# Kernel optimization log

Hardware: AMD Instinct MI355X
Metric: run time of the kernel (lower is better)

## Reference

```python
import jax, jax.numpy as jnp
import numpy as np
import math

EMBED_DIM = 1024
N_HEADS = 16
HEAD_DIM = EMBED_DIM // N_HEADS
B, N = 2, 2048


def setup_inputs() -> dict:
    key = jax.random.key(0)
    k1, k2, k3 = jax.random.split(key, 3)
    x = jax.random.normal(k1, (B, N, EMBED_DIM), dtype=jnp.float32)
    # Per-head Linear(D, 3*head_dim), stacked over heads. PyTorch Linear init scale ~1/sqrt(fan_in).
    bound = 1.0 / math.sqrt(EMBED_DIM)
    Wkqv = jax.random.uniform(k2, (N_HEADS, EMBED_DIM, 3 * HEAD_DIM), dtype=jnp.float32, minval=-bound, maxval=bound)
    bkqv = jax.random.uniform(k3, (N_HEADS, 3 * HEAD_DIM), dtype=jnp.float32, minval=-bound, maxval=bound)
    return {"x": x, "Wkqv": Wkqv, "bkqv": bkqv}


def reference(x, Wkqv, bkqv):
    Bx, Nx, D = x.shape
    hd = Wkqv.shape[-1] // 3
    # all heads at once: [B, H, N, 3*hd]
    proj = jnp.einsum('bnd,hdf->bhnf', x, Wkqv) + bkqv[None, :, None, :]
    # torch.split order in the original is (k, q, v)
    k, q, v = jnp.split(proj, 3, axis=-1)
    # scores = q @ k^T / sqrt(head_dim)   [B, H, N, N]
    scores = jnp.einsum('bhqd,bhkd->bhqk', q, k) / math.sqrt(hd)
    causal = jnp.tril(jnp.ones((Nx, Nx), dtype=bool))
    scores = jnp.where(causal[None, None, :, :], scores, -jnp.inf)
    attn = jax.nn.softmax(scores, axis=-1)
    out = jnp.einsum('bhqk,bhkd->bhqd', attn, v)  # [B, H, N, hd]
    # concat heads -> [B, N, D]  (forward() passes no out_matrix, so no output projection)
    return out.transpose(0, 2, 1, 3).reshape(Bx, Nx, D)
```

## Files before the change

kernel.cpp:

```cpp
#include <hip/hip_runtime.h>
#include <math.h>

typedef float f32x4 __attribute__((ext_vector_type(4)));
typedef __bf16 bf16x8 __attribute__((ext_vector_type(8)));

#define MFMA16(a, b, c) __builtin_amdgcn_mfma_f32_16x16x32_bf16((a), (b), (c), 0, 0, 0)

constexpr int Bsz = 2, Nseq = 2048, Dm = 1024, Hh = 16, HDim = 64, F3 = 192;
constexpr int Mrows = Bsz * Nseq;
constexpr int NC = Hh * F3;
constexpr float QSCALE = 0.125f * 1.4426950408889634f;

__device__ inline void load_lds16(const void* g, void* l) {
    __builtin_amdgcn_global_load_lds((const __attribute__((address_space(1))) void*)g,
                                     (__attribute__((address_space(3))) void*)l, 16, 0, 0);
}

#define FENCE asm volatile("" ::: "memory")
#define BARRIER do { FENCE; __builtin_amdgcn_s_barrier(); FENCE; } while (0)
#define WAIT6 asm volatile("s_waitcnt vmcnt(6)" ::: "memory")

__global__ __launch_bounds__(256) void conv_x_kernel(const float* __restrict__ x,
                                                     __bf16* __restrict__ xb) {
    int i = blockIdx.x * 256 + threadIdx.x;
    const float4* xv = reinterpret_cast<const float4*>(x);
    float4 a = xv[2 * i];
    float4 b = xv[2 * i + 1];
    bf16x8 o = {(__bf16)a.x, (__bf16)a.y, (__bf16)a.z, (__bf16)a.w,
                (__bf16)b.x, (__bf16)b.y, (__bf16)b.z, (__bf16)b.w};
    *reinterpret_cast<bf16x8*>(xb + 8 * i) = o;
}

__global__ __launch_bounds__(256) void conv_w_kernel(const float* __restrict__ w,
                                                     __bf16* __restrict__ wt) {
    __shared__ __bf16 tile[32][66];
    int h = blockIdx.z, d0 = blockIdx.x * 32, c0 = blockIdx.y * 64;
    for (int i = threadIdx.x; i < 32 * 64; i += 256) {
        int di = i >> 6, cj = i & 63;
        tile[di][cj] = (__bf16)w[(size_t)(h * Dm + d0 + di) * F3 + c0 + cj];
    }
    __syncthreads();
    for (int i = threadIdx.x; i < 32 * 64; i += 256) {
        int ci = i >> 5, dj = i & 31;
        wt[(size_t)(h * F3 + c0 + ci) * Dm + d0 + dj] = tile[dj][ci];
    }
}

__global__ __launch_bounds__(512, 2) void gemm_proj(const __bf16* __restrict__ xb,
                                                    const __bf16* __restrict__ wt,
                                                    const float* __restrict__ bias,
                                                    __bf16* __restrict__ kbuf,
                                                    __bf16* __restrict__ qbuf,
                                                    __bf16* __restrict__ vt) {
    __shared__ __align__(16) __bf16 Ab[2][256 * 64];
    __shared__ __align__(16) __bf16 Bb[2][256 * 64];

    int flat = blockIdx.x;
    int swz = (flat & 7) * 24 + (flat >> 3);
    int bm = swz / 12, bn = swz % 12;
    int r0 = bm * 256, n0 = bn * 256;

    int w = threadIdx.x >> 6, lane = threadIdx.x & 63;
    int col = lane & 15, quad = lane >> 4;
    int wm = w >> 2, wn = w & 3;

    f32x4 acc[8][4] = {};
    bf16x8 af[2][4];
    bf16x8 bfr[2][2];

    auto stageA = [&](int t, int s, int h) {
        int rl = lane >> 3;
        int cg = (lane & 7) ^ rl;
#pragma unroll
        for (int r = 0; r < 2; r++) {
            int rowb = r * 128 + h * 64 + w * 8;
            load_lds16(xb + (size_t)(r0 + rowb + rl) * Dm + t * 64 + cg * 8,
                       &Ab[s][rowb * 64]);
        }
    };
    auto stageB = [&](int t, int s, int h) {
        int rl = lane >> 3;
        int cg = (lane & 7) ^ rl;
#pragma unroll
        for (int r = 0; r < 2; r++) {
            int rowb = ((w >> 2) + r * 2) * 64 + h * 32 + (w & 3) * 8;
            load_lds16(wt + (size_t)(n0 + rowb + rl) * Dm + t * 64 + cg * 8,
                       &Bb[s][rowb * 64]);
        }
    };

    auto readA = [&](int s, int mh) {
#pragma unroll
        for (int ks = 0; ks < 2; ks++)
#pragma unroll
            for (int mt = 0; mt < 4; mt++) {
                int row = wm * 128 + mh * 64 + mt * 16 + col;
                af[ks][mt] = *reinterpret_cast<const bf16x8*>(
                    &Ab[s][row * 64 + (((ks * 4 + quad) ^ (row & 7)) * 8)]);
            }
    };
    auto readB = [&](int s, int nh) {
#pragma unroll
        for (int ks = 0; ks < 2; ks++)
#pragma unroll
            for (int nt = 0; nt < 2; nt++) {
                int row = wn * 64 + nh * 32 + nt * 16 + col;
                bfr[ks][nt] = *reinterpret_cast<const bf16x8*>(
                    &Bb[s][row * 64 + (((ks * 4 + quad) ^ (row & 7)) * 8)]);
            }
    };
    auto mfmaQ = [&](int mh, int nh) {
        __builtin_amdgcn_s_setprio(1);
#pragma unroll
        for (int ks = 0; ks < 2; ks++)
#pragma unroll
            for (int mt = 0; mt < 4; mt++)
#pragma unroll
                for (int nt = 0; nt < 2; nt++)
                    acc[mh * 4 + mt][nh * 2 + nt] =
                        MFMA16(af[ks][mt], bfr[ks][nt], acc[mh * 4 + mt][nh * 2 + nt]);
        __builtin_amdgcn_s_setprio(0);
    };

    stageA(0, 0, 0); stageB(0, 0, 0); stageA(0, 0, 1); stageB(0, 0, 1);
    stageA(1, 1, 0);
    stageB(1, 1, 0); stageA(1, 1, 1);
    WAIT6;
    BARRIER;

    for (int i = 0; i < 8; i++) {
        int t0 = 2 * i;
        int t2 = t0 + 2; if (t2 > 15) t2 = 15;
        int t3 = t0 + 3; if (t3 > 15) t3 = 15;

        readA(0, 0); readB(0, 0);
        stageB(t0 + 1, 1, 1);
        BARRIER; mfmaQ(0, 0); BARRIER;

        readB(0, 1);
        stageA(t2, 0, 0);
        BARRIER; mfmaQ(0, 1); BARRIER;

        readA(0, 1); readB(0, 0);
        BARRIER; mfmaQ(1, 0); BARRIER;

        readB(0, 1);
        stageB(t2, 0, 0); stageA(t2, 0, 1);
        WAIT6;
        BARRIER; mfmaQ(1, 1); BARRIER;

        readA(1, 0); readB(1, 0);
        stageB(t2, 0, 1);
        BARRIER; mfmaQ(0, 0); BARRIER;

        readB(1, 1);
        stageA(t3, 1, 0);
        BARRIER; mfmaQ(0, 1); BARRIER;

        readA(1, 1); readB(1, 0);
        BARRIER; mfmaQ(1, 0); BARRIER;

        readB(1, 1);
        stageB(t3, 1, 0); stageA(t3, 1, 1);
        WAIT6;
        BARRIER; mfmaQ(1, 1); BARRIER;
    }

#pragma unroll
    for (int nt = 0; nt < 4; nt++) {
        int g = n0 + wn * 64 + nt * 16 + col;
        int h = g / F3, c = g - h * F3;
        float bv = bias[g];
        bool isq = (c >= 64 && c < 128), isv = (c >= 128);
        int cd = c & 63;
#pragma unroll
        for (int mt = 0; mt < 8; mt++) {
#pragma unroll
            for (int rg = 0; rg < 4; rg++) {
                int r = r0 + wm * 128 + mt * 16 + quad * 4 + rg;
                int b = r >> 11, n = r & (Nseq - 1);
                float v = acc[mt][nt][rg] + bv;
                if (isq) v *= QSCALE;
                size_t bh = (size_t)(b * Hh + h);
                if (isv) vt[(bh * HDim + cd) * Nseq + n] = (__bf16)v;
                else ((isq) ? qbuf : kbuf)[(bh * Nseq + n) * HDim + cd] = (__bf16)v;
            }
        }
    }
}

__global__ __launch_bounds__(256) void proj_small(const float* __restrict__ x,
                                                  const __bf16* __restrict__ wt,
                                                  const float* __restrict__ bias,
                                                  __bf16* __restrict__ kbuf,
                                                  __bf16* __restrict__ qbuf,
                                                  __bf16* __restrict__ vt) {
    int h = blockIdx.y;
    int wave = threadIdx.x >> 6, lane = threadIdx.x & 63;
    int col = lane & 15, quad = lane >> 4;
    int r0 = blockIdx.x * 128 + wave * 32;

    f32x4 acc[12][2] = {};
    const float* xr0 = x + (size_t)(r0 + col) * Dm + quad * 8;
    const float* xr1 = xr0 + 16 * Dm;
    const __bf16* wbase = wt + (size_t)(h * F3 + col) * Dm + quad * 8;

    for (int k0 = 0; k0 < Dm; k0 += 32) {
        float4 a0lo = *reinterpret_cast<const float4*>(xr0 + k0);
        float4 a0hi = *reinterpret_cast<const float4*>(xr0 + k0 + 4);
        float4 a1lo = *reinterpret_cast<const float4*>(xr1 + k0);
        float4 a1hi = *reinterpret_cast<const float4*>(xr1 + k0 + 4);
        bf16x8 a0 = {(__bf16)a0lo.x, (__bf16)a0lo.y, (__bf16)a0lo.z, (__bf16)a0lo.w,
                     (__bf16)a0hi.x, (__bf16)a0hi.y, (__bf16)a0hi.z, (__bf16)a0hi.w};
        bf16x8 a1 = {(__bf16)a1lo.x, (__bf16)a1lo.y, (__bf16)a1lo.z, (__bf16)a1lo.w,
                     (__bf16)a1hi.x, (__bf16)a1hi.y, (__bf16)a1hi.z, (__bf16)a1hi.w};
#pragma unroll
        for (int ct = 0; ct < 12; ct++) {
            bf16x8 bf = *reinterpret_cast<const bf16x8*>(wbase + ct * 16 * Dm + k0);
            acc[ct][0] = MFMA16(a0, bf, acc[ct][0]);
            acc[ct][1] = MFMA16(a1, bf, acc[ct][1]);
        }
    }
#pragma unroll
    for (int ct = 0; ct < 12; ct++) {
        int c = ct * 16 + col;
        float bv = bias[h * F3 + c];
        int cd = c & 63;
        bool isq = (c >= 64 && c < 128), isv = (c >= 128);
#pragma unroll
        for (int rt = 0; rt < 2; rt++) {
#pragma unroll
            for (int rg = 0; rg < 4; rg++) {
                int r = r0 + rt * 16 + quad * 4 + rg;
                int b = r >> 11, n = r & (Nseq - 1);
                float v = acc[ct][rt][rg] + bv;
                if (isq) v *= QSCALE;
                size_t bh = (size_t)(b * Hh + h);
                if (isv) vt[(bh * HDim + cd) * Nseq + n] = (__bf16)v;
                else ((isq) ? qbuf : kbuf)[(bh * Nseq + n) * HDim + cd] = (__bf16)v;
            }
        }
    }
}

__global__ __launch_bounds__(512) void attn_kernel(const __bf16* __restrict__ qbuf,
                                                   const __bf16* __restrict__ kbuf,
                                                   const __bf16* __restrict__ vt,
                                                   float* __restrict__ out) {
    __shared__ __align__(16) __bf16 Kb[64 * 64];
    __shared__ __align__(16) __bf16 Vb[64 * 64];
    __shared__ __align__(16) __bf16 plds[8][16][72];
    int bh = blockIdx.x;
    int b = bh >> 4, h = bh & 15;
    int pair = blockIdx.y;
    int wave = threadIdx.x >> 6, lane = threadIdx.x & 63;
    int col = lane & 15, quad = lane >> 4;
    int tile = (wave < 4) ? pair : (31 - pair);
    int q0 = tile * 64 + (wave & 3) * 16;

    const __bf16* qbase = qbuf + (size_t)bh * Nseq * HDim;
    const __bf16* kbase = kbuf + (size_t)bh * Nseq * HDim;
    const __bf16* vbase = vt + (size_t)bh * HDim * Nseq;

    bf16x8 aq0 = *reinterpret_cast<const bf16x8*>(qbase + (q0 + col) * HDim + quad * 8);
    bf16x8 aq1 = *reinterpret_cast<const bf16x8*>(qbase + (q0 + col) * HDim + quad * 8 + 32);

    f32x4 o[4] = {};
    float lsum[4] = {0.f, 0.f, 0.f, 0.f};

    int mb = q0 & ~63;
    int loop_end = 2048 - 64 * pair;

    int srow = threadIdx.x >> 3;
    int schunk = (threadIdx.x & 7) ^ (srow & 7);
    const __bf16* ksrc0 = kbase + srow * HDim + schunk * 8;
    const __bf16* vsrc0 = vbase + (size_t)srow * Nseq + schunk * 8;
    __bf16* kdst = Kb + wave * 512;
    __bf16* vdst = Vb + wave * 512;

    int sw0 = ((quad ^ (col & 7)) * 8);
    int sw1 = (((quad + 4) ^ (col & 7)) * 8);

    for (int kb = 0; kb < loop_end; kb += 64) {
        __syncthreads();
        load_lds16(ksrc0 + kb * HDim, kdst);
        load_lds16(vsrc0 + kb, vdst);
        __syncthreads();

        if (kb <= mb) {
            bool masked = (kb == mb);
            f32x4 z = {};
            f32x4 s[4];
#pragma unroll
            for (int g = 0; g < 4; g++) {
                const __bf16* krow = Kb + (col + 16 * g) * 64;
                bf16x8 k0 = *reinterpret_cast<const bf16x8*>(krow + sw0);
                bf16x8 k1 = *reinterpret_cast<const bf16x8*>(krow + sw1);
                s[g] = MFMA16(aq0, k0, z);
                s[g] = MFMA16(aq1, k1, s[g]);
            }
            if (masked) {
#pragma unroll
                for (int g = 0; g < 4; g++) {
#pragma unroll
                    for (int r = 0; r < 4; r++) {
                        int qi = q0 + quad * 4 + r;
                        float p = (kb + col + 16 * g <= qi) ? exp2f(s[g][r]) : 0.f;
                        lsum[r] += p;
                        plds[wave][quad * 4 + r][col + 16 * g] = (__bf16)p;
                    }
                }
            } else {
#pragma unroll
                for (int g = 0; g < 4; g++) {
#pragma unroll
                    for (int r = 0; r < 4; r++) {
                        float p = exp2f(s[g][r]);
                        lsum[r] += p;
                        plds[wave][quad * 4 + r][col + 16 * g] = (__bf16)p;
                    }
                }
            }
            bf16x8 pa0 = *reinterpret_cast<const bf16x8*>(&plds[wave][col][quad * 8]);
            bf16x8 pa1 = *reinterpret_cast<const bf16x8*>(&plds[wave][col][32 + quad * 8]);
#pragma unroll
            for (int nt = 0; nt < 4; nt++) {
                const __bf16* vrow = Vb + (col + 16 * nt) * 64;
                bf16x8 v0 = *reinterpret_cast<const bf16x8*>(vrow + sw0);
                bf16x8 v1 = *reinterpret_cast<const bf16x8*>(vrow + sw1);
                o[nt] = MFMA16(pa0, v0, o[nt]);
                o[nt] = MFMA16(pa1, v1, o[nt]);
            }
        }
    }

    float linv[4];
#pragma unroll
    for (int r = 0; r < 4; r++) {
        float s = lsum[r];
        s += __shfl_xor(s, 1);
        s += __shfl_xor(s, 2);
        s += __shfl_xor(s, 4);
        s += __shfl_xor(s, 8);
        linv[r] = 1.f / s;
    }
#pragma unroll
    for (int nt = 0; nt < 4; nt++) {
#pragma unroll
        for (int r = 0; r < 4; r++) {
            int qi = q0 + quad * 4 + r;
            out[((size_t)(b * Nseq + qi)) * Dm + h * HDim + nt * 16 + col] = o[nt][r] * linv[r];
        }
    }
}

extern "C" void kernel_launch(void* const* d_in, const int* in_sizes, int n_in,
                              void* d_out, int out_size, void* d_ws, size_t ws_size,
                              hipStream_t stream) {
    const float* x = nullptr;
    const float* w = nullptr;
    const float* bias = nullptr;
    for (int i = 0; i < n_in; i++) {
        if (in_sizes[i] == Mrows * Dm) x = (const float*)d_in[i];
        else if (in_sizes[i] == Hh * Dm * F3) w = (const float*)d_in[i];
        else if (in_sizes[i] == Hh * F3) bias = (const float*)d_in[i];
    }
    float* outp = (float*)d_out;

    char* ws = (char*)d_ws;
    __bf16* wt = (__bf16*)(ws);
    __bf16* kbuf = (__bf16*)(ws + 6291456);
    __bf16* qbuf = (__bf16*)(ws + 6291456 + 8388608);
    __bf16* vt = (__bf16*)(ws + 6291456 + 2 * 8388608);
    __bf16* xb = (__bf16*)(ws + 6291456 + 3 * 8388608);

    conv_w_kernel<<<dim3(Dm / 32, F3 / 64, Hh), 256, 0, stream>>>(w, wt);
    if (ws_size >= (size_t)(6291456 + 4 * 8388608)) {
        conv_x_kernel<<<Mrows * Dm / (8 * 256), 256, 0, stream>>>(x, xb);
        gemm_proj<<<dim3(Mrows / 256 * (NC / 256)), 512, 0, stream>>>(xb, wt, bias, kbuf, qbuf, vt);
    } else {
        proj_small<<<dim3(Mrows / 128, Hh), 256, 0, stream>>>(x, wt, bias, kbuf, qbuf, vt);
    }
    attn_kernel<<<dim3(32, 16), 512, 0, stream>>>(qbuf, kbuf, vt, outp);
}
```

Measured before the change: 172.0 us.

## Double-buffer K/V tiles in LDS to overlap global loads with attention compute

Adds a second LDS buffer for the K and V tiles and prefetches the next tile with global_load_lds while the current tile is processed. Explicit vmcnt waits and raw barriers replace the two __syncthreads per iteration, so memory latency can be hidden behind the MFMA and exp work. The cost is doubled LDS for K/V, which may lower occupancy, and there is still one barrier at the end of each iteration.

```diff
diff --git a/kernel.cpp b/kernel.cpp
--- a/kernel.cpp
+++ b/kernel.cpp
@@ -247,8 +247,8 @@
                                                    const __bf16* __restrict__ kbuf,
                                                    const __bf16* __restrict__ vt,
                                                    float* __restrict__ out) {
-    __shared__ __align__(16) __bf16 Kb[64 * 64];
-    __shared__ __align__(16) __bf16 Vb[64 * 64];
+    __shared__ __align__(16) __bf16 Kb[2][64 * 64];
+    __shared__ __align__(16) __bf16 Vb[2][64 * 64];
     __shared__ __align__(16) __bf16 plds[8][16][72];
     int bh = blockIdx.x;
     int b = bh >> 4, h = bh & 15;
@@ -275,29 +275,39 @@
     int schunk = (threadIdx.x & 7) ^ (srow & 7);
     const __bf16* ksrc0 = kbase + srow * HDim + schunk * 8;
     const __bf16* vsrc0 = vbase + (size_t)srow * Nseq + schunk * 8;
-    __bf16* kdst = Kb + wave * 512;
-    __bf16* vdst = Vb + wave * 512;
 
     int sw0 = ((quad ^ (col & 7)) * 8);
     int sw1 = (((quad + 4) ^ (col & 7)) * 8);
 
+    load_lds16(ksrc0, &Kb[0][wave * 512]);
+    load_lds16(vsrc0, &Vb[0][wave * 512]);
+    FENCE;
+
+    int s = 0;
     for (int kb = 0; kb < loop_end; kb += 64) {
-        __syncthreads();
-        load_lds16(ksrc0 + kb * HDim, kdst);
-        load_lds16(vsrc0 + kb, vdst);
-        __syncthreads();
+        int nkb = kb + 64;
+        if (nkb < loop_end) {
+            load_lds16(ksrc0 + nkb * HDim, &Kb[s ^ 1][wave * 512]);
+            load_lds16(vsrc0 + nkb, &Vb[s ^ 1][wave * 512]);
+            asm volatile("s_waitcnt vmcnt(2)" ::: "memory");
+        } else {
+            asm volatile("s_waitcnt vmcnt(0)" ::: "memory");
+        }
+        BARRIER;
 
         if (kb <= mb) {
             bool masked = (kb == mb);
+            const __bf16* Kcur = Kb[s];
+            const __bf16* Vcur = Vb[s];
             f32x4 z = {};
-            f32x4 s[4];
+            f32x4 sc[4];
 #pragma unroll
             for (int g = 0; g < 4; g++) {
-                const __bf16* krow = Kb + (col + 16 * g) * 64;
+                const __bf16* krow = Kcur + (col + 16 * g) * 64;
                 bf16x8 k0 = *reinterpret_cast<const bf16x8*>(krow + sw0);
                 bf16x8 k1 = *reinterpret_cast<const bf16x8*>(krow + sw1);
-                s[g] = MFMA16(aq0, k0, z);
-                s[g] = MFMA16(aq1, k1, s[g]);
+                sc[g] = MFMA16(aq0, k0, z);
+                sc[g] = MFMA16(aq1, k1, sc[g]);
             }
             if (masked) {
 #pragma unroll
@@ -305,7 +315,7 @@
 #pragma unroll
                     for (int r = 0; r < 4; r++) {
                         int qi = q0 + quad * 4 + r;
-                        float p = (kb + col + 16 * g <= qi) ? exp2f(s[g][r]) : 0.f;
+                        float p = (kb + col + 16 * g <= qi) ? exp2f(sc[g][r]) : 0.f;
                         lsum[r] += p;
                         plds[wave][quad * 4 + r][col + 16 * g] = (__bf16)p;
                     }
@@ -315,7 +325,7 @@
                 for (int g = 0; g < 4; g++) {
 #pragma unroll
                     for (int r = 0; r < 4; r++) {
-                        float p = exp2f(s[g][r]);
+                        float p = exp2f(sc[g][r]);
                         lsum[r] += p;
                         plds[wave][quad * 4 + r][col + 16 * g] = (__bf16)p;
                     }
@@ -325,24 +335,26 @@
             bf16x8 pa1 = *reinterpret_cast<const bf16x8*>(&plds[wave][col][32 + quad * 8]);
 #pragma unroll
             for (int nt = 0; nt < 4; nt++) {
-                const __bf16* vrow = Vb + (col + 16 * nt) * 64;
+                const __bf16* vrow = Vcur + (col + 16 * nt) * 64;
                 bf16x8 v0 = *reinterpret_cast<const bf16x8*>(vrow + sw0);
                 bf16x8 v1 = *reinterpret_cast<const bf16x8*>(vrow + sw1);
                 o[nt] = MFMA16(pa0, v0, o[nt]);
                 o[nt] = MFMA16(pa1, v1, o[nt]);
             }
         }
+        BARRIER;
+        s ^= 1;
     }
 
     float linv[4];
 #pragma unroll
     for (int r = 0; r < 4; r++) {
-        float s = lsum[r];
-        s += __shfl_xor(s, 1);
-        s += __shfl_xor(s, 2);
-        s += __shfl_xor(s, 4);
-        s += __shfl_xor(s, 8);
-        linv[r] = 1.f / s;
+        float t = lsum[r];
+        t += __shfl_xor(t, 1);
+        t += __shfl_xor(t, 2);
+        t += __shfl_xor(t, 4);
+        t += __shfl_xor(t, 8);
+        linv[r] = 1.f / t;
     }
 #pragma unroll
     for (int nt = 0; nt < 4; nt++) {
```

Measured after the change: 171.1 us. Within noise of the previous version (-0.5%).
